# Kernel tuning notes

Measured on AMD Instinct MI355X. Metric: run time of the kernel, lower is better.

Reference implementation:

```python
import jax, jax.numpy as jnp
import numpy as np

N = 20000       # total atoms
E = 320000      # edges (avg degree 16)
F = 128         # num_features
R = 32          # num_radial
NB = 3          # num_blocks
CUTOFF = 5.0
MAX_Z = 37      # max_atomic_number + 1
MIN_DIST = 0.3
PI = 3.141592653589793


def swish(x):
    return x * jax.nn.sigmoid(x)


def sph_harm_l2(rhat):
    # Real spherical harmonics lmax=2, e3nn ordering, 'component' normalization.
    x, y, z = rhat[:, 0], rhat[:, 1], rhat[:, 2]
    s3, s5, s15 = 1.7320508075688772, 2.23606797749979, 3.872983346207417
    sh1 = jnp.stack([s3 * y, s3 * z, s3 * x], axis=-1)                    # l=1 (odd)
    sh2 = jnp.stack([s15 * x * y, s15 * y * z, 0.5 * s5 * (3.0 * z * z - 1.0),
                     s15 * z * x, 0.5 * s15 * (x * x - y * y)], axis=-1)  # l=2 (even)
    return sh1, sh2


def setup_inputs() -> dict:
    key = jax.random.key(0)
    ks = jax.random.split(key, 16)
    rn = lambda k, shape, scale: jax.random.normal(k, shape, dtype=jnp.float32) * scale
    inp = {}
    inp["z"] = jax.random.randint(ks[0], (N,), 0, MAX_Z)
    inp["pos"] = rn(ks[1], (N, 3), 3.0)
    inp["edge_index"] = jax.random.randint(ks[2], (2, E), 0, N)
    # embedding params
    inp["emb_table"] = rn(ks[3], (MAX_Z, F), 1.0)
    inp["emb_W"] = rn(ks[4], (F, F), F ** -0.5)
    inp["emb_b"] = jnp.zeros((F,), jnp.float32)
    # trainable Bessel frequencies (init n*pi, as in bessel RBF)
    inp["bessel_freq"] = jnp.arange(1, R + 1, dtype=jnp.float32) * PI
    # per-block params, stacked over NB blocks
    inp["Wf1"] = rn(ks[5], (NB, R, F), R ** -0.5)
    inp["bf1"] = jnp.zeros((NB, F), jnp.float32)
    inp["Wf2"] = rn(ks[6], (NB, F, 4 * F), F ** -0.5)
    inp["Wsrc"] = rn(ks[7], (NB, F, F), F ** -0.5)
    inp["Wu"] = rn(ks[8], (NB, F, 3 * F), F ** -0.5)
    inp["W1o"] = rn(ks[9], (NB, F, F), F ** -0.5)
    inp["W1e"] = rn(ks[10], (NB, F, F), F ** -0.5)
    inp["W2e"] = rn(ks[11], (NB, F, F), F ** -0.5)
    inp["Wup"] = rn(ks[12], (NB, 4 * F, F), (4 * F) ** -0.5)
    return inp


def forward(z, pos, edge_index, emb_table, emb_W, emb_b, bessel_freq,
            Wf1, bf1, Wf2, Wsrc, Wu, W1o, W1e, W2e, Wup):
    i, j = edge_index[0], edge_index[1]
    rij = pos[j] - pos[i]                                   # [E,3]
    r = jnp.sqrt(jnp.sum(rij * rij, axis=-1) + 1e-12)       # [E]
    rhat = rij / (r[:, None] + 1e-6)
    # mask replaces the edge filtering (min_distance and radius cutoff)
    edge_mask = ((r >= MIN_DIST) & (r < CUTOFF)).astype(pos.dtype)
    sh1, sh2 = sph_harm_l2(rhat)                            # [E,3], [E,5]
    # trainable Bessel RBF with cosine cutoff envelope
    fc = 0.5 * (jnp.cos(PI * r / CUTOFF) + 1.0) * edge_mask
    rbf = jnp.sqrt(2.0 / CUTOFF) * jnp.sin(bessel_freq[None, :] * r[:, None] / CUTOFF) / (r[:, None] + 1e-6)
    rbf = rbf * fc[:, None]                                 # [E,R]
    # atom embedding
    S = swish(emb_table[z] @ emb_W + emb_b)                 # [N,F]
    T = jnp.zeros((N, 11, F), S.dtype)                      # 1o(3)+1e(3)+2e(5) x F channels
    for b in range(NB):
        # radial filter network -> per-edge gates
        w = swish(rbf @ Wf1[b] + bf1[b]) @ Wf2[b]           # [E,4F]
        w = w * edge_mask[:, None]
        wS, w1, w2, w3 = jnp.split(w, 4, axis=-1)
        Sj = S[j]                                           # [E,F] gather
        # scalar messages
        mS = wS * swish(Sj @ Wsrc[b])                       # [E,F]
        aggS = jax.ops.segment_sum(mS, i, num_segments=N)   # [N,F]
        # equivariant messages: sh(l) outer-product edge features
        u1, u2, u3 = jnp.split(Sj @ Wu[b], 3, axis=-1)
        m1o = sh1[:, :, None] * (w1 * u1)[:, None, :]       # [E,3,F]
        m1e = sh1[:, :, None] * (w2 * u2)[:, None, :]       # [E,3,F]
        m2e = sh2[:, :, None] * (w3 * u3)[:, None, :]       # [E,5,F]
        mT = jnp.concatenate([m1o, m1e, m2e], axis=1)       # [E,11,F]
        aggT = jax.ops.segment_sum(mT, i, num_segments=N)   # [N,11,F] scatter-add
        Tin = T + aggT
        # per-irrep channel mixing (self-interaction)
        T1o = jnp.einsum('nmf,fg->nmg', Tin[:, 0:3], W1o[b])
        T1e = jnp.einsum('nmf,fg->nmg', Tin[:, 3:6], W1e[b])
        T2e = jnp.einsum('nmf,fg->nmg', Tin[:, 6:11], W2e[b])
        T = jnp.concatenate([T1o, T1e, T2e], axis=1)
        # invariant norms of each irrep feed back into scalar track
        inv = jnp.concatenate([jnp.sum(T1o * T1o, 1), jnp.sum(T1e * T1e, 1),
                               jnp.sum(T2e * T2e, 1)], axis=-1)   # [N,3F]
        S = S + swish(jnp.concatenate([aggS, inv], axis=-1) @ Wup[b])
    return S, T.reshape(N, 11 * F)


def reference(z, pos, edge_index, emb_table, emb_W, emb_b, bessel_freq,
              Wf1, bf1, Wf2, Wsrc, Wu, W1o, W1e, W2e, Wup):
    return forward(z, pos, edge_index, emb_table, emb_W, emb_b, bessel_freq,
                   Wf1, bf1, Wf2, Wsrc, Wu, W1o, W1e, W2e, Wup)
```

## Files before the change

kernel.cpp:

```cpp
#include <hip/hip_runtime.h>
#include <cstdint>
#include <cstddef>

#define NN 20000
#define EE 320000
#define FF 128
#define RR 32
#define MTE 16

typedef float  f32x4  __attribute__((ext_vector_type(4)));
typedef short  bf16x8 __attribute__((ext_vector_type(8)));

__device__ __forceinline__ float swishf(float x) {
    return x / (1.f + __expf(-x));
}
__device__ __forceinline__ unsigned short f2bf(float f) {
    unsigned int u = __builtin_bit_cast(unsigned int, f);
    u = (u + 0x7FFFu + ((u >> 16) & 1u)) >> 16;
    return (unsigned short)u;
}
__device__ __forceinline__ float bf2f(unsigned short h) {
    unsigned int u = ((unsigned int)h) << 16;
    return __builtin_bit_cast(float, u);
}

__global__ __launch_bounds__(256) void geom_deg_kernel(
    const float* __restrict__ pos, const int* __restrict__ eidx,
    int* __restrict__ deg)
{
    int e = blockIdx.x * 256 + threadIdx.x;
    if (e >= EE) return;
    int i = eidx[e], j = eidx[EE + e];
    float dx = pos[3*j+0] - pos[3*i+0];
    float dy = pos[3*j+1] - pos[3*i+1];
    float dz = pos[3*j+2] - pos[3*i+2];
    float r = sqrtf(dx*dx + dy*dy + dz*dz + 1e-12f);
    if (r >= 0.3f && r < 5.0f) atomicAdd(&deg[i], 1);
}

__global__ __launch_bounds__(256) void scan_kernel(
    const int* __restrict__ deg, int* __restrict__ cursor, int* __restrict__ cnt)
{
    __shared__ int part[256];
    const int t = threadIdx.x;
    const int lo = t * 79;
    const int hi = min(lo + 79, NN);
    int s = 0;
    for (int k = lo; k < hi; k++) s += deg[k];
    part[t] = s;
    __syncthreads();
    for (int off = 1; off < 256; off <<= 1) {
        int v = (t >= off) ? part[t - off] : 0;
        __syncthreads();
        part[t] += v;
        __syncthreads();
    }
    int run = (t == 0) ? 0 : part[t - 1];
    for (int k = lo; k < hi; k++) { cursor[k] = run; run += deg[k]; }
    if (t == 255) cnt[0] = part[255];
}

__global__ __launch_bounds__(256) void geom_scatter_kernel(
    const float* __restrict__ pos, const int* __restrict__ eidx,
    const float* __restrict__ freq, int* __restrict__ cursor,
    int* __restrict__ ei, int* __restrict__ ej,
    float* __restrict__ sh, unsigned short* __restrict__ rbfq)
{
    int e = blockIdx.x * 256 + threadIdx.x;
    if (e >= EE) return;
    int i = eidx[e], j = eidx[EE + e];
    float dx = pos[3*j+0] - pos[3*i+0];
    float dy = pos[3*j+1] - pos[3*i+1];
    float dz = pos[3*j+2] - pos[3*i+2];
    float r = sqrtf(dx*dx + dy*dy + dz*dz + 1e-12f);
    if (!(r >= 0.3f && r < 5.0f)) return;
    int slot = atomicAdd(&cursor[i], 1);
    ei[slot] = i; ej[slot] = j;
    float ir = 1.f / (r + 1e-6f);
    float x = dx*ir, y = dy*ir, z = dz*ir;
    const float s3 = 1.7320508075688772f, s5 = 2.23606797749979f, s15 = 3.872983346207417f;
    float* shp = sh + (size_t)slot * 8;
    shp[0] = s3*y; shp[1] = s3*z; shp[2] = s3*x;
    shp[3] = s15*x*y; shp[4] = s15*y*z; shp[5] = 0.5f*s5*(3.f*z*z - 1.f);
    shp[6] = s15*z*x; shp[7] = 0.5f*s15*(x*x - y*y);
    float fc = 0.5f * (cosf(3.14159265358979323846f * r * 0.2f) + 1.f);
    float pref = 0.6324555320336759f * fc * ir;
    unsigned short* rp = rbfq + (size_t)slot * RR;
    for (int k = 0; k < RR; k++) rp[k] = f2bf(pref * sinf(freq[k] * r * 0.2f));
}

__global__ __launch_bounds__(128) void embed_kernel(
    const int* __restrict__ z, const float* __restrict__ emb_table,
    const float* __restrict__ emb_W, const float* __restrict__ emb_b,
    float* __restrict__ S)
{
    int n = blockIdx.x;
    int f = threadIdx.x;
    __shared__ float row[FF];
    row[f] = emb_table[(size_t)z[n]*FF + f];
    __syncthreads();
    float acc = emb_b[f];
    for (int k = 0; k < FF; k++) acc += row[k] * emb_W[k*FF + f];
    S[(size_t)n*FF + f] = swishf(acc);
}

__global__ __launch_bounds__(256) void pack_kernel(
    const float* __restrict__ W1o, const float* __restrict__ W1e,
    const float* __restrict__ W2e, const float* __restrict__ Wup,
    unsigned short* __restrict__ ph, unsigned short* __restrict__ pl)
{
    int t = blockIdx.x * 256 + threadIdx.x;
    if (t >= 3 * 14336) return;
    int b = t / 14336, r = t % 14336;
    const float* src; int nks; size_t dstoff;
    if (r < 6144) {
        int mat = r / 2048, rr = r % 2048;
        src = (mat == 0 ? W1o : mat == 1 ? W1e : W2e) + (size_t)b * 16384;
        nks = 4;
        dstoff = (size_t)b * 114688 + (size_t)mat * 16384 + (size_t)rr * 8;
        r = rr;
    } else {
        int rr = r - 6144;
        src = Wup + (size_t)b * 65536;
        nks = 16;
        dstoff = (size_t)b * 114688 + 49152 + (size_t)rr * 8;
        r = rr;
    }
    int lane = r & 63;
    int fi = r >> 6;
    int ks = fi % nks, ct = fi / nks;
    int col = ct * 16 + (lane & 15);
    int kb = ks * 32 + (lane >> 4) * 8;
    #pragma unroll
    for (int e = 0; e < 8; e++) {
        float v = src[(size_t)(kb + e) * 128 + col];
        unsigned short h = f2bf(v);
        ph[dstoff + e] = h;
        pl[dstoff + e] = f2bf(v - bf2f(h));
    }
}

__global__ __launch_bounds__(256) void pack_pu_kernel(
    const float* __restrict__ Wsrc, const float* __restrict__ Wu,
    unsigned short* __restrict__ packPU)
{
    int t = blockIdx.x * 256 + threadIdx.x;
    if (t >= 3 * 8192) return;
    int b = t / 8192, r = t % 8192;
    int lane = r & 63, fi = r >> 6;
    int ks = fi & 3, ct = fi >> 2;
    int kb = ks * 32 + (lane >> 4) * 8;
    int colq = lane & 15;
    const float* src; int col, stride;
    if (ct < 8) { src = Wsrc + (size_t)b * 16384; col = ct*16 + colq; stride = 128; }
    else        { src = Wu   + (size_t)b * 49152; col = (ct-8)*16 + colq; stride = 384; }
    size_t dst = (size_t)b * 65536 + (size_t)fi * 512 + (size_t)lane * 8;
    #pragma unroll
    for (int e = 0; e < 8; e++)
        packPU[dst + e] = f2bf(src[(size_t)(kb + e) * stride + col]);
}

__global__ __launch_bounds__(256) void pack_f2_kernel(
    const float* __restrict__ Wf2, unsigned short* __restrict__ packF2)
{
    int t = blockIdx.x * 256 + threadIdx.x;
    if (t >= 3 * 8192) return;
    int b = t / 8192, r = t % 8192;
    int lane = r & 63, fi = r >> 6;
    int ks = fi & 3, ct = fi >> 2;
    int kb = ks * 32 + (lane >> 4) * 8;
    int col = ct * 16 + (lane & 15);
    const float* src = Wf2 + (size_t)b * 65536;
    size_t dst = (size_t)b * 65536 + (size_t)fi * 512 + (size_t)lane * 8;
    #pragma unroll
    for (int e = 0; e < 8; e++)
        packF2[dst + e] = f2bf(src[(size_t)(kb + e) * 512 + col]);
}

__global__ __launch_bounds__(256) void proj_kernel(
    const float* __restrict__ S, const unsigned short* __restrict__ packPU,
    unsigned short* __restrict__ PU)
{
    __shared__ float stage[16][132];
    const int tid = threadIdx.x;
    const int n0 = blockIdx.x * 16;

    for (int idx = tid; idx < 512; idx += 256) {
        int row = idx >> 5, k4 = (idx & 31) << 2;
        *(float4*)&stage[row][k4] = *(const float4*)&S[((size_t)(n0 + row) << 7) + k4];
    }
    __syncthreads();

    const int lane = tid & 63;
    const int wid  = tid >> 6;
    const int row  = lane & 15;
    const int k0   = (lane >> 4) * 8;

    f32x4 acc[8];
    #pragma unroll
    for (int c = 0; c < 8; c++) acc[c] = (f32x4){0.f, 0.f, 0.f, 0.f};

    #pragma unroll
    for (int ks = 0; ks < 4; ks++) {
        const float* sp = &stage[row][ks*32 + k0];
        bf16x8 a;
        #pragma unroll
        for (int e = 0; e < 8; e++) a[e] = (short)f2bf(sp[e]);
        #pragma unroll
        for (int cti = 0; cti < 8; cti++) {
            int ct = wid * 8 + cti;
            bf16x8 b = *(const bf16x8*)(packPU + (((size_t)ct * 4 + ks) * 64 + lane) * 8);
            acc[cti] = __builtin_amdgcn_mfma_f32_16x16x32_bf16(a, b, acc[cti], 0, 0, 0);
        }
    }

    #pragma unroll
    for (int cti = 0; cti < 8; cti++) {
        int ct = wid * 8 + cti;
        int col = ct * 16 + (lane & 15);
        #pragma unroll
        for (int q = 0; q < 4; q++) {
            int n = n0 + (lane >> 4) * 4 + q;
            float v = acc[cti][q];
            if (ct < 8) v = swishf(v);
            PU[(size_t)n * 512 + col] = f2bf(v);
        }
    }
}

__global__ __launch_bounds__(256) void msg_kernel(
    const int* __restrict__ cnt,
    const int* __restrict__ ei, const int* __restrict__ ej,
    const float* __restrict__ sh, const unsigned short* __restrict__ rbfq,
    const float* __restrict__ Wf1, const float* __restrict__ bf1,
    const unsigned short* __restrict__ packF2, const unsigned short* __restrict__ PU,
    float* __restrict__ aggS, float* __restrict__ aggT)
{
    const int Ea = cnt[0];
    const int base = blockIdx.x * MTE;
    if (base >= Ea) return;
    const int nval = min(MTE, Ea - base);
    const int tid = threadIdx.x;

    __shared__ float          rbf_s[MTE][RR];
    __shared__ unsigned short h_s[MTE][FF];
    __shared__ unsigned short w_s[MTE][512];
    __shared__ float          sh_s[MTE][8];
    __shared__ int            i_s[MTE];
    __shared__ int            j_s[MTE];

    if (tid < MTE) {
        i_s[tid] = (tid < nval) ? ei[base + tid] : -1;
        j_s[tid] = (tid < nval) ? ej[base + tid] : 0;
    }
    if (tid >= 64 && tid < 64 + MTE*8) {
        int t = tid - 64, e = t >> 3;
        sh_s[e][t & 7] = (e < nval) ? sh[(size_t)(base + e)*8 + (t & 7)] : 0.f;
    }
    for (int t = tid; t < MTE*RR; t += 256) {
        int e = t >> 5, k = t & 31;
        rbf_s[e][k] = (e < nval) ? bf2f(rbfq[(size_t)(base + e)*RR + k]) : 0.f;
    }
    __syncthreads();

    {
        const int f = tid & 127, eh = tid >> 7;
        float hacc[8];
        float bb = bf1[f];
        #pragma unroll
        for (int k = 0; k < 8; k++) hacc[k] = bb;
        for (int r = 0; r < RR; r++) {
            float wv = Wf1[r*FF + f];
            #pragma unroll
            for (int k = 0; k < 8; k++) hacc[k] += rbf_s[eh*8 + k][r] * wv;
        }
        #pragma unroll
        for (int k = 0; k < 8; k++) h_s[eh*8 + k][f] = f2bf(swishf(hacc[k]));
    }
    __syncthreads();

    {
        const int lane = tid & 63;
        const int wid  = tid >> 6;
        const int ra   = lane & 15;
        const int k0   = (lane >> 4) * 8;
        f32x4 acc[8];
        #pragma unroll
        for (int c = 0; c < 8; c++) acc[c] = (f32x4){0.f, 0.f, 0.f, 0.f};
        #pragma unroll
        for (int ks = 0; ks < 4; ks++) {
            bf16x8 a = *(const bf16x8*)&h_s[ra][ks*32 + k0];
            #pragma unroll
            for (int cti = 0; cti < 8; cti++) {
                int ct = wid * 8 + cti;
                bf16x8 b = *(const bf16x8*)(packF2 + (((size_t)ct * 4 + ks) * 64 + lane) * 8);
                acc[cti] = __builtin_amdgcn_mfma_f32_16x16x32_bf16(a, b, acc[cti], 0, 0, 0);
            }
        }
        #pragma unroll
        for (int cti = 0; cti < 8; cti++) {
            int ct = wid * 8 + cti;
            int col = ct * 16 + (lane & 15);
            #pragma unroll
            for (int q = 0; q < 4; q++)
                w_s[(lane >> 4)*4 + q][col] = f2bf(acc[cti][q]);
        }
    }
    __syncthreads();

    const int f = tid & 127;
    if (tid < 128) {
        float aS = 0.f, a3 = 0.f, a4 = 0.f, a5 = 0.f;
        int cur = i_s[0];
        for (int e = 0; e < nval; e++) {
            int ie = i_s[e];
            if (ie != cur) {
                atomicAdd(&aggS[((size_t)cur << 7) + f], aS);
                size_t bT = (((size_t)cur*11 + 3) << 7) + f;
                atomicAdd(&aggT[bT], a3); atomicAdd(&aggT[bT + 128], a4); atomicAdd(&aggT[bT + 256], a5);
                aS = a3 = a4 = a5 = 0.f; cur = ie;
            }
            const unsigned short* pu = PU + (size_t)j_s[e] * 512;
            float wS = bf2f(w_s[e][f]),       P  = bf2f(pu[f]);
            float w2 = bf2f(w_s[e][256 + f]), U2 = bf2f(pu[256 + f]);
            aS += wS * P;
            float v = w2 * U2;
            a3 += sh_s[e][0]*v; a4 += sh_s[e][1]*v; a5 += sh_s[e][2]*v;
        }
        atomicAdd(&aggS[((size_t)cur << 7) + f], aS);
        size_t bT = (((size_t)cur*11 + 3) << 7) + f;
        atomicAdd(&aggT[bT], a3); atomicAdd(&aggT[bT + 128], a4); atomicAdd(&aggT[bT + 256], a5);
    } else {
        float a0 = 0.f, a1 = 0.f, a2 = 0.f;
        float a6 = 0.f, a7 = 0.f, a8 = 0.f, a9 = 0.f, a10 = 0.f;
        int cur = i_s[0];
        for (int e = 0; e < nval; e++) {
            int ie = i_s[e];
            if (ie != cur) {
                size_t bT = (((size_t)cur*11) << 7) + f;
                atomicAdd(&aggT[bT], a0); atomicAdd(&aggT[bT + 128], a1); atomicAdd(&aggT[bT + 256], a2);
                size_t bT2 = (((size_t)cur*11 + 6) << 7) + f;
                atomicAdd(&aggT[bT2], a6); atomicAdd(&aggT[bT2 + 128], a7); atomicAdd(&aggT[bT2 + 256], a8);
                atomicAdd(&aggT[bT2 + 384], a9); atomicAdd(&aggT[bT2 + 512], a10);
                a0 = a1 = a2 = a6 = a7 = a8 = a9 = a10 = 0.f; cur = ie;
            }
            const unsigned short* pu = PU + (size_t)j_s[e] * 512;
            float w1 = bf2f(w_s[e][128 + f]), U1 = bf2f(pu[128 + f]);
            float w3 = bf2f(w_s[e][384 + f]), U3 = bf2f(pu[384 + f]);
            float v1 = w1 * U1;
            a0 += sh_s[e][0]*v1; a1 += sh_s[e][1]*v1; a2 += sh_s[e][2]*v1;
            float v3 = w3 * U3;
            a6 += sh_s[e][3]*v3; a7 += sh_s[e][4]*v3; a8 += sh_s[e][5]*v3;
            a9 += sh_s[e][6]*v3; a10 += sh_s[e][7]*v3;
        }
        size_t bT = (((size_t)cur*11) << 7) + f;
        atomicAdd(&aggT[bT], a0); atomicAdd(&aggT[bT + 128], a1); atomicAdd(&aggT[bT + 256], a2);
        size_t bT2 = (((size_t)cur*11 + 6) << 7) + f;
        atomicAdd(&aggT[bT2], a6); atomicAdd(&aggT[bT2 + 128], a7); atomicAdd(&aggT[bT2 + 256], a8);
        atomicAdd(&aggT[bT2 + 384], a9); atomicAdd(&aggT[bT2 + 512], a10);
    }
}

template<int GSIZE>
__global__ __launch_bounds__(256) void tgemm_kernel(
    const float* __restrict__ aggT,
    const unsigned short* __restrict__ Wh, const unsigned short* __restrict__ Wl,
    float* __restrict__ T, float* __restrict__ inv,
    int goff, int invoff, int addT)
{
    __shared__ float stage[GSIZE][16][132];
    const int tid = threadIdx.x;
    const int n0 = blockIdx.x * 16;

    const int total = GSIZE * 16 * 32;
    for (int idx = tid; idx < total; idx += 256) {
        int mg  = idx >> 9;
        int rem = idx & 511;
        int row = rem >> 5;
        int k4  = (rem & 31) << 2;
        size_t g = (((size_t)(n0 + row) * 11 + goff + mg) << 7) + k4;
        float4 v = *(const float4*)&aggT[g];
        if (addT) {
            float4 tv = *(const float4*)&T[g];
            v.x += tv.x; v.y += tv.y; v.z += tv.z; v.w += tv.w;
        }
        *(float4*)&stage[mg][row][k4] = v;
    }
    __syncthreads();

    const int lane = tid & 63;
    const int wid  = tid >> 6;
    const int row  = lane & 15;
    const int k0   = (lane >> 4) * 8;

    f32x4 acc[GSIZE][2];
    #pragma unroll
    for (int mg = 0; mg < GSIZE; mg++) {
        acc[mg][0] = (f32x4){0.f, 0.f, 0.f, 0.f};
        acc[mg][1] = (f32x4){0.f, 0.f, 0.f, 0.f};
    }

    #pragma unroll
    for (int ks = 0; ks < 4; ks++) {
        bf16x8 ah[GSIZE], al[GSIZE];
        #pragma unroll
        for (int mg = 0; mg < GSIZE; mg++) {
            const float* sp = &stage[mg][row][ks*32 + k0];
            float v0[4], v1[4];
            *(float4*)v0 = *(const float4*)sp;
            *(float4*)v1 = *(const float4*)(sp + 4);
            #pragma unroll
            for (int e = 0; e < 4; e++) {
                unsigned short h0 = f2bf(v0[e]);
                ah[mg][e]   = (short)h0;
                al[mg][e]   = (short)f2bf(v0[e] - bf2f(h0));
                unsigned short h1 = f2bf(v1[e]);
                ah[mg][4+e] = (short)h1;
                al[mg][4+e] = (short)f2bf(v1[e] - bf2f(h1));
            }
        }
        #pragma unroll
        for (int cti = 0; cti < 2; cti++) {
            const int ct = wid * 2 + cti;
            size_t boff = (((size_t)ct * 4 + ks) * 64 + lane) * 8;
            bf16x8 bh = *(const bf16x8*)(Wh + boff);
            bf16x8 bl = *(const bf16x8*)(Wl + boff);
            #pragma unroll
            for (int mg = 0; mg < GSIZE; mg++) {
                acc[mg][cti] = __builtin_amdgcn_mfma_f32_16x16x32_bf16(ah[mg], bh, acc[mg][cti], 0, 0, 0);
                acc[mg][cti] = __builtin_amdgcn_mfma_f32_16x16x32_bf16(al[mg], bh, acc[mg][cti], 0, 0, 0);
                acc[mg][cti] = __builtin_amdgcn_mfma_f32_16x16x32_bf16(ah[mg], bl, acc[mg][cti], 0, 0, 0);
            }
        }
    }

    #pragma unroll
    for (int cti = 0; cti < 2; cti++) {
        const int ct = wid * 2 + cti;
        const int fc = ct * 16 + (lane & 15);
        #pragma unroll
        for (int q = 0; q < 4; q++) {
            const int n = n0 + (lane >> 4) * 4 + q;
            float iv = 0.f;
            #pragma unroll
            for (int mg = 0; mg < GSIZE; mg++) {
                float o = acc[mg][cti][q];
                T[(((size_t)n * 11 + goff + mg) << 7) + fc] = o;
                iv += o * o;
            }
            inv[(size_t)n * 384 + invoff + fc] = iv;
        }
    }
}

__global__ __launch_bounds__(256) void sgemm2_kernel(
    const float* __restrict__ aggS, const float* __restrict__ inv,
    const unsigned short* __restrict__ Wh, const unsigned short* __restrict__ Wl,
    float* __restrict__ S)
{
    __shared__ float stage[16][516];
    const int tid = threadIdx.x;
    const int n0 = blockIdx.x * 16;

    for (int idx = tid; idx < 16 * 128; idx += 256) {
        int row = idx >> 7;
        int k4  = (idx & 127) << 2;
        float4 v;
        if (k4 < 128) v = *(const float4*)&aggS[((size_t)(n0 + row) << 7) + k4];
        else          v = *(const float4*)&inv[(size_t)(n0 + row) * 384 + (k4 - 128)];
        *(float4*)&stage[row][k4] = v;
    }
    __syncthreads();

    const int lane = tid & 63;
    const int wid  = tid >> 6;
    const int row  = lane & 15;
    const int k0   = (lane >> 4) * 8;

    f32x4 acc[2];
    acc[0] = (f32x4){0.f, 0.f, 0.f, 0.f};
    acc[1] = (f32x4){0.f, 0.f, 0.f, 0.f};

    for (int ks = 0; ks < 16; ks++) {
        const float* sp = &stage[row][ks*32 + k0];
        float v0[4], v1[4];
        *(float4*)v0 = *(const float4*)sp;
        *(float4*)v1 = *(const float4*)(sp + 4);
        bf16x8 ah, al;
        #pragma unroll
        for (int e = 0; e < 4; e++) {
            unsigned short h0 = f2bf(v0[e]);
            ah[e]   = (short)h0;
            al[e]   = (short)f2bf(v0[e] - bf2f(h0));
            unsigned short h1 = f2bf(v1[e]);
            ah[4+e] = (short)h1;
            al[4+e] = (short)f2bf(v1[e] - bf2f(h1));
        }
        #pragma unroll
        for (int cti = 0; cti < 2; cti++) {
            const int ct = wid * 2 + cti;
            size_t boff = (((size_t)ct * 16 + ks) * 64 + lane) * 8;
            bf16x8 bh = *(const bf16x8*)(Wh + boff);
            bf16x8 bl = *(const bf16x8*)(Wl + boff);
            acc[cti] = __builtin_amdgcn_mfma_f32_16x16x32_bf16(ah, bh, acc[cti], 0, 0, 0);
            acc[cti] = __builtin_amdgcn_mfma_f32_16x16x32_bf16(al, bh, acc[cti], 0, 0, 0);
            acc[cti] = __builtin_amdgcn_mfma_f32_16x16x32_bf16(ah, bl, acc[cti], 0, 0, 0);
        }
    }

    #pragma unroll
    for (int cti = 0; cti < 2; cti++) {
        const int ct = wid * 2 + cti;
        const int fc = ct * 16 + (lane & 15);
        #pragma unroll
        for (int q = 0; q < 4; q++) {
            const int n = n0 + (lane >> 4) * 4 + q;
            size_t o = ((size_t)n << 7) + fc;
            S[o] += swishf(acc[cti][q]);
        }
    }
}

extern "C" void kernel_launch(void* const* d_in, const int* in_sizes, int n_in,
                              void* d_out, int out_size, void* d_ws, size_t ws_size,
                              hipStream_t stream)
{
    const int*   z         = (const int*)  d_in[0];
    const float* pos       = (const float*)d_in[1];
    const int*   eidx      = (const int*)  d_in[2];
    const float* emb_table = (const float*)d_in[3];
    const float* emb_W     = (const float*)d_in[4];
    const float* emb_b     = (const float*)d_in[5];
    const float* freq      = (const float*)d_in[6];
    const float* Wf1       = (const float*)d_in[7];
    const float* bf1       = (const float*)d_in[8];
    const float* Wf2       = (const float*)d_in[9];
    const float* Wsrc      = (const float*)d_in[10];
    const float* Wu        = (const float*)d_in[11];
    const float* W1o       = (const float*)d_in[12];
    const float* W1e       = (const float*)d_in[13];
    const float* W2e       = (const float*)d_in[14];
    const float* Wup       = (const float*)d_in[15];

    float* S = (float*)d_out;
    float* T = S + (size_t)NN*FF;

    char* w = (char*)d_ws;
    int*   cnt    = (int*)w;                      w += 256;
    int*   deg    = (int*)w;                      w += (size_t)NN*4 + 128;
    int*   cursor = (int*)w;                      w += (size_t)NN*4 + 128;
    int*   ei     = (int*)w;                      w += (size_t)EE*4;
    int*   ej     = (int*)w;                      w += (size_t)EE*4;
    float* sh     = (float*)w;                    w += (size_t)EE*8*4;
    unsigned short* rbfq = (unsigned short*)w;    w += (size_t)EE*RR*2;
    unsigned short* PU   = (unsigned short*)w;    w += (size_t)NN*512*2;
    float* aggS   = (float*)w;                    w += (size_t)NN*FF*4;
    float* aggT   = (float*)w;                    w += (size_t)NN*11*FF*4;
    float* inv    = (float*)w;                    w += (size_t)NN*384*4;
    unsigned short* packH  = (unsigned short*)w;  w += (size_t)344064*2;
    unsigned short* packL  = (unsigned short*)w;  w += (size_t)344064*2;
    unsigned short* packPU = (unsigned short*)w;  w += (size_t)3*65536*2;
    unsigned short* packF2 = (unsigned short*)w;  w += (size_t)3*65536*2;

    hipMemsetAsync(deg, 0, (size_t)NN*4, stream);

    geom_deg_kernel<<<(EE + 255)/256, 256, 0, stream>>>(pos, eidx, deg);
    scan_kernel<<<1, 256, 0, stream>>>(deg, cursor, cnt);
    geom_scatter_kernel<<<(EE + 255)/256, 256, 0, stream>>>(pos, eidx, freq, cursor, ei, ej, sh, rbfq);
    embed_kernel<<<NN, 128, 0, stream>>>(z, emb_table, emb_W, emb_b, S);
    pack_kernel<<<(3*14336 + 255)/256, 256, 0, stream>>>(W1o, W1e, W2e, Wup, packH, packL);
    pack_pu_kernel<<<(3*8192 + 255)/256, 256, 0, stream>>>(Wsrc, Wu, packPU);
    pack_f2_kernel<<<(3*8192 + 255)/256, 256, 0, stream>>>(Wf2, packF2);

    for (int b = 0; b < 3; b++) {
        hipMemsetAsync(aggS, 0, (size_t)NN*FF*4 + (size_t)NN*11*FF*4, stream);
        proj_kernel<<<NN/16, 256, 0, stream>>>(S, packPU + (size_t)b*65536, PU);
        msg_kernel<<<(EE + MTE - 1)/MTE, 256, 0, stream>>>(
            cnt, ei, ej, sh, rbfq,
            Wf1 + (size_t)b*RR*FF, bf1 + (size_t)b*FF,
            packF2 + (size_t)b*65536, PU, aggS, aggT);

        const unsigned short* H = packH + (size_t)b*114688;
        const unsigned short* L = packL + (size_t)b*114688;
        tgemm_kernel<3><<<NN/16, 256, 0, stream>>>(aggT, H +     0, L +     0, T, inv, 0,   0, b > 0);
        tgemm_kernel<3><<<NN/16, 256, 0, stream>>>(aggT, H + 16384, L + 16384, T, inv, 3, 128, b > 0);
        tgemm_kernel<5><<<NN/16, 256, 0, stream>>>(aggT, H + 32768, L + 32768, T, inv, 6, 256, b > 0);
        sgemm2_kernel<<<NN/16, 256, 0, stream>>>(aggS, inv, H + 49152, L + 49152, S);
    }
}
```

Measured before the change: 985.2 us.

## Segment edges per destination node, replace atomics with stores, fuse projection into sgemm2

The message kernel now assigns each block a fixed group of destination nodes through a CSR start array and walks only their sorted edges. Each node's sum is built in registers and written with plain stores, which removes the float atomics and the per-block memset of the aggregation buffers. Nodes with no edges are zeroed explicitly. PU is stored interleaved (four values per feature) so one 8-byte load fetches all four, and the next block's source projection is fused into sgemm2's epilogue, dropping the separate proj launches. The risk is load imbalance, since blocks with high-degree nodes loop longer, and fewer blocks run overall.

```diff
diff --git a/kernel.cpp b/kernel.cpp
--- a/kernel.cpp
+++ b/kernel.cpp
@@ -7,6 +7,7 @@
 #define FF 128
 #define RR 32
 #define MTE 16
+#define NPB 4
 
 typedef float  f32x4  __attribute__((ext_vector_type(4)));
 typedef short  bf16x8 __attribute__((ext_vector_type(8)));
@@ -39,7 +40,7 @@
 }
 
 __global__ __launch_bounds__(256) void scan_kernel(
-    const int* __restrict__ deg, int* __restrict__ cursor, int* __restrict__ cnt)
+    const int* __restrict__ deg, int* __restrict__ cursor, int* __restrict__ cstart)
 {
     __shared__ int part[256];
     const int t = threadIdx.x;
@@ -56,8 +57,8 @@
         __syncthreads();
     }
     int run = (t == 0) ? 0 : part[t - 1];
-    for (int k = lo; k < hi; k++) { cursor[k] = run; run += deg[k]; }
-    if (t == 255) cnt[0] = part[255];
+    for (int k = lo; k < hi; k++) { cursor[k] = run; cstart[k] = run; run += deg[k]; }
+    if (t == 255) cstart[NN] = run;
 }
 
 __global__ __launch_bounds__(256) void geom_scatter_kernel(
@@ -217,147 +218,177 @@
     #pragma unroll
     for (int cti = 0; cti < 8; cti++) {
         int ct = wid * 8 + cti;
-        int col = ct * 16 + (lane & 15);
+        int cblk = ct >> 3;
+        int fcol = (ct & 7) * 16 + (lane & 15);
         #pragma unroll
         for (int q = 0; q < 4; q++) {
             int n = n0 + (lane >> 4) * 4 + q;
             float v = acc[cti][q];
-            if (ct < 8) v = swishf(v);
-            PU[(size_t)n * 512 + col] = f2bf(v);
+            if (cblk == 0) v = swishf(v);
+            PU[(size_t)n * 512 + fcol * 4 + cblk] = f2bf(v);
         }
     }
 }
 
 __global__ __launch_bounds__(256) void msg_kernel(
-    const int* __restrict__ cnt,
+    const int* __restrict__ cstart,
     const int* __restrict__ ei, const int* __restrict__ ej,
     const float* __restrict__ sh, const unsigned short* __restrict__ rbfq,
     const float* __restrict__ Wf1, const float* __restrict__ bf1,
     const unsigned short* __restrict__ packF2, const unsigned short* __restrict__ PU,
     float* __restrict__ aggS, float* __restrict__ aggT)
 {
-    const int Ea = cnt[0];
-    const int base = blockIdx.x * MTE;
-    if (base >= Ea) return;
-    const int nval = min(MTE, Ea - base);
+    const int n0 = blockIdx.x * NPB;
+    const int estart = cstart[n0];
+    const int eend   = cstart[n0 + NPB];
     const int tid = threadIdx.x;
+    const int f = tid & 127;
+    const int half = tid >> 7;
+    const int lane = tid & 63;
+    const int wid  = tid >> 6;
 
     __shared__ float          rbf_s[MTE][RR];
     __shared__ unsigned short h_s[MTE][FF];
-    __shared__ unsigned short w_s[MTE][512];
+    __shared__ unsigned short w_s[MTE][520];
     __shared__ float          sh_s[MTE][8];
-    __shared__ int            i_s[MTE];
-    __shared__ int            j_s[MTE];
-
-    if (tid < MTE) {
-        i_s[tid] = (tid < nval) ? ei[base + tid] : -1;
-        j_s[tid] = (tid < nval) ? ej[base + tid] : 0;
-    }
-    if (tid >= 64 && tid < 64 + MTE*8) {
-        int t = tid - 64, e = t >> 3;
-        sh_s[e][t & 7] = (e < nval) ? sh[(size_t)(base + e)*8 + (t & 7)] : 0.f;
-    }
-    for (int t = tid; t < MTE*RR; t += 256) {
-        int e = t >> 5, k = t & 31;
-        rbf_s[e][k] = (e < nval) ? bf2f(rbfq[(size_t)(base + e)*RR + k]) : 0.f;
-    }
-    __syncthreads();
-
-    {
-        const int f = tid & 127, eh = tid >> 7;
-        float hacc[8];
-        float bb = bf1[f];
-        #pragma unroll
-        for (int k = 0; k < 8; k++) hacc[k] = bb;
-        for (int r = 0; r < RR; r++) {
-            float wv = Wf1[r*FF + f];
-            #pragma unroll
-            for (int k = 0; k < 8; k++) hacc[k] += rbf_s[eh*8 + k][r] * wv;
-        }
-        #pragma unroll
-        for (int k = 0; k < 8; k++) h_s[eh*8 + k][f] = f2bf(swishf(hacc[k]));
-    }
-    __syncthreads();
-
-    {
-        const int lane = tid & 63;
-        const int wid  = tid >> 6;
-        const int ra   = lane & 15;
-        const int k0   = (lane >> 4) * 8;
-        f32x4 acc[8];
-        #pragma unroll
-        for (int c = 0; c < 8; c++) acc[c] = (f32x4){0.f, 0.f, 0.f, 0.f};
-        #pragma unroll
-        for (int ks = 0; ks < 4; ks++) {
-            bf16x8 a = *(const bf16x8*)&h_s[ra][ks*32 + k0];
+    __shared__ int            i_s[MTE], j_s[MTE];
+
+    float aS=0.f, a3=0.f, a4=0.f, a5=0.f;
+    float a0=0.f,a1=0.f,a2=0.f,a6=0.f,a7=0.f,a8=0.f,a9=0.f,a10=0.f;
+    int cur = -1;
+
+    for (int eoff = estart; eoff < eend; eoff += MTE) {
+        const int te = min(MTE, eend - eoff);
+        __syncthreads();
+        if (tid < MTE) {
+            i_s[tid] = (tid < te) ? ei[eoff + tid] : -1;
+            j_s[tid] = (tid < te) ? ej[eoff + tid] : 0;
+        }
+        if (tid >= 64 && tid < 64 + MTE*8) {
+            int t = tid - 64, e = t >> 3;
+            sh_s[e][t & 7] = (e < te) ? sh[(size_t)(eoff + e)*8 + (t & 7)] : 0.f;
+        }
+        for (int t = tid; t < MTE*RR; t += 256) {
+            int e = t >> 5, k = t & 31;
+            rbf_s[e][k] = (e < te) ? bf2f(rbfq[(size_t)(eoff + e)*RR + k]) : 0.f;
+        }
+        __syncthreads();
+        if (cur < 0) cur = i_s[0];
+
+        {
+            float hacc[8];
+            float bb = bf1[f];
+            #pragma unroll
+            for (int k = 0; k < 8; k++) hacc[k] = bb;
+            for (int r = 0; r < RR; r++) {
+                float wv = Wf1[r*FF + f];
+                #pragma unroll
+                for (int k = 0; k < 8; k++) hacc[k] += rbf_s[half*8 + k][r] * wv;
+            }
+            #pragma unroll
+            for (int k = 0; k < 8; k++)
+                h_s[half*8 + k][f] = f2bf(swishf(hacc[k]));
+        }
+        __syncthreads();
+
+        {
+            const int ra = lane & 15, k0 = (lane >> 4) * 8;
+            f32x4 wacc[8];
+            #pragma unroll
+            for (int c = 0; c < 8; c++) wacc[c] = (f32x4){0.f, 0.f, 0.f, 0.f};
+            #pragma unroll
+            for (int ks = 0; ks < 4; ks++) {
+                bf16x8 a = *(const bf16x8*)&h_s[ra][ks*32 + k0];
+                #pragma unroll
+                for (int cti = 0; cti < 8; cti++) {
+                    int ct = wid * 8 + cti;
+                    bf16x8 b = *(const bf16x8*)(packF2 + (((size_t)ct * 4 + ks) * 64 + lane) * 8);
+                    wacc[cti] = __builtin_amdgcn_mfma_f32_16x16x32_bf16(a, b, wacc[cti], 0, 0, 0);
+                }
+            }
             #pragma unroll
             for (int cti = 0; cti < 8; cti++) {
                 int ct = wid * 8 + cti;
-                bf16x8 b = *(const bf16x8*)(packF2 + (((size_t)ct * 4 + ks) * 64 + lane) * 8);
-                acc[cti] = __builtin_amdgcn_mfma_f32_16x16x32_bf16(a, b, acc[cti], 0, 0, 0);
-            }
-        }
-        #pragma unroll
-        for (int cti = 0; cti < 8; cti++) {
-            int ct = wid * 8 + cti;
-            int col = ct * 16 + (lane & 15);
-            #pragma unroll
-            for (int q = 0; q < 4; q++)
-                w_s[(lane >> 4)*4 + q][col] = f2bf(acc[cti][q]);
-        }
-    }
-    __syncthreads();
-
-    const int f = tid & 127;
-    if (tid < 128) {
-        float aS = 0.f, a3 = 0.f, a4 = 0.f, a5 = 0.f;
-        int cur = i_s[0];
-        for (int e = 0; e < nval; e++) {
+                int cblk = ct >> 3;
+                int fcol = (ct & 7) * 16 + (lane & 15);
+                #pragma unroll
+                for (int q = 0; q < 4; q++)
+                    w_s[(lane >> 4)*4 + q][fcol*4 + cblk] = f2bf(wacc[cti][q]);
+            }
+        }
+        __syncthreads();
+
+        uint2 puv[MTE];
+        #pragma unroll
+        for (int e = 0; e < MTE; e++)
+            puv[e] = *(const uint2*)(PU + ((size_t)j_s[e] << 9) + (f << 2));
+
+        #pragma unroll
+        for (int e = 0; e < MTE; e++) {
+            if (e >= te) break;
             int ie = i_s[e];
             if (ie != cur) {
-                atomicAdd(&aggS[((size_t)cur << 7) + f], aS);
-                size_t bT = (((size_t)cur*11 + 3) << 7) + f;
-                atomicAdd(&aggT[bT], a3); atomicAdd(&aggT[bT + 128], a4); atomicAdd(&aggT[bT + 256], a5);
-                aS = a3 = a4 = a5 = 0.f; cur = ie;
-            }
-            const unsigned short* pu = PU + (size_t)j_s[e] * 512;
-            float wS = bf2f(w_s[e][f]),       P  = bf2f(pu[f]);
-            float w2 = bf2f(w_s[e][256 + f]), U2 = bf2f(pu[256 + f]);
-            aS += wS * P;
-            float v = w2 * U2;
-            a3 += sh_s[e][0]*v; a4 += sh_s[e][1]*v; a5 += sh_s[e][2]*v;
-        }
-        atomicAdd(&aggS[((size_t)cur << 7) + f], aS);
-        size_t bT = (((size_t)cur*11 + 3) << 7) + f;
-        atomicAdd(&aggT[bT], a3); atomicAdd(&aggT[bT + 128], a4); atomicAdd(&aggT[bT + 256], a5);
-    } else {
-        float a0 = 0.f, a1 = 0.f, a2 = 0.f;
-        float a6 = 0.f, a7 = 0.f, a8 = 0.f, a9 = 0.f, a10 = 0.f;
-        int cur = i_s[0];
-        for (int e = 0; e < nval; e++) {
-            int ie = i_s[e];
-            if (ie != cur) {
-                size_t bT = (((size_t)cur*11) << 7) + f;
-                atomicAdd(&aggT[bT], a0); atomicAdd(&aggT[bT + 128], a1); atomicAdd(&aggT[bT + 256], a2);
-                size_t bT2 = (((size_t)cur*11 + 6) << 7) + f;
-                atomicAdd(&aggT[bT2], a6); atomicAdd(&aggT[bT2 + 128], a7); atomicAdd(&aggT[bT2 + 256], a8);
-                atomicAdd(&aggT[bT2 + 384], a9); atomicAdd(&aggT[bT2 + 512], a10);
-                a0 = a1 = a2 = a6 = a7 = a8 = a9 = a10 = 0.f; cur = ie;
-            }
-            const unsigned short* pu = PU + (size_t)j_s[e] * 512;
-            float w1 = bf2f(w_s[e][128 + f]), U1 = bf2f(pu[128 + f]);
-            float w3 = bf2f(w_s[e][384 + f]), U3 = bf2f(pu[384 + f]);
-            float v1 = w1 * U1;
-            a0 += sh_s[e][0]*v1; a1 += sh_s[e][1]*v1; a2 += sh_s[e][2]*v1;
-            float v3 = w3 * U3;
-            a6 += sh_s[e][3]*v3; a7 += sh_s[e][4]*v3; a8 += sh_s[e][5]*v3;
-            a9 += sh_s[e][6]*v3; a10 += sh_s[e][7]*v3;
-        }
-        size_t bT = (((size_t)cur*11) << 7) + f;
-        atomicAdd(&aggT[bT], a0); atomicAdd(&aggT[bT + 128], a1); atomicAdd(&aggT[bT + 256], a2);
-        size_t bT2 = (((size_t)cur*11 + 6) << 7) + f;
-        atomicAdd(&aggT[bT2], a6); atomicAdd(&aggT[bT2 + 128], a7); atomicAdd(&aggT[bT2 + 256], a8);
-        atomicAdd(&aggT[bT2 + 384], a9); atomicAdd(&aggT[bT2 + 512], a10);
+                if (half == 0) {
+                    aggS[((size_t)cur << 7) + f] = aS;
+                    size_t bT = (((size_t)cur*11 + 3) << 7) + f;
+                    aggT[bT] = a3; aggT[bT + 128] = a4; aggT[bT + 256] = a5;
+                    aS = a3 = a4 = a5 = 0.f;
+                } else {
+                    size_t bT = (((size_t)cur*11) << 7) + f;
+                    aggT[bT] = a0; aggT[bT + 128] = a1; aggT[bT + 256] = a2;
+                    size_t bT2 = (((size_t)cur*11 + 6) << 7) + f;
+                    aggT[bT2] = a6; aggT[bT2 + 128] = a7; aggT[bT2 + 256] = a8;
+                    aggT[bT2 + 384] = a9; aggT[bT2 + 512] = a10;
+                    a0=a1=a2=a6=a7=a8=a9=a10=0.f;
+                }
+                cur = ie;
+            }
+            uint2 wv2 = *(const uint2*)&w_s[e][f*4];
+            uint2 pv  = puv[e];
+            if (half == 0) {
+                float wS = bf2f((unsigned short)(wv2.x & 0xffff));
+                float w2 = bf2f((unsigned short)(wv2.y & 0xffff));
+                float P  = bf2f((unsigned short)(pv.x  & 0xffff));
+                float U2 = bf2f((unsigned short)(pv.y  & 0xffff));
+                aS += wS * P;
+                float v = w2 * U2;
+                a3 += sh_s[e][0]*v; a4 += sh_s[e][1]*v; a5 += sh_s[e][2]*v;
+            } else {
+                float w1 = bf2f((unsigned short)(wv2.x >> 16));
+                float w3 = bf2f((unsigned short)(wv2.y >> 16));
+                float U1 = bf2f((unsigned short)(pv.x  >> 16));
+                float U3 = bf2f((unsigned short)(pv.y  >> 16));
+                float v1 = w1 * U1;
+                a0 += sh_s[e][0]*v1; a1 += sh_s[e][1]*v1; a2 += sh_s[e][2]*v1;
+                float v3 = w3 * U3;
+                a6 += sh_s[e][3]*v3; a7 += sh_s[e][4]*v3; a8 += sh_s[e][5]*v3;
+                a9 += sh_s[e][6]*v3; a10 += sh_s[e][7]*v3;
+            }
+        }
+    }
+    if (cur >= 0) {
+        if (half == 0) {
+            aggS[((size_t)cur << 7) + f] = aS;
+            size_t bT = (((size_t)cur*11 + 3) << 7) + f;
+            aggT[bT] = a3; aggT[bT + 128] = a4; aggT[bT + 256] = a5;
+        } else {
+            size_t bT = (((size_t)cur*11) << 7) + f;
+            aggT[bT] = a0; aggT[bT + 128] = a1; aggT[bT + 256] = a2;
+            size_t bT2 = (((size_t)cur*11 + 6) << 7) + f;
+            aggT[bT2] = a6; aggT[bT2 + 128] = a7; aggT[bT2 + 256] = a8;
+            aggT[bT2 + 384] = a9; aggT[bT2 + 512] = a10;
+        }
+    }
+    #pragma unroll
+    for (int ln = 0; ln < NPB; ln++) {
+        int n = n0 + ln;
+        if (cstart[n + 1] == cstart[n]) {
+            for (int idx = tid; idx < 12*128; idx += 256) {
+                int row = idx >> 7, ff = idx & 127;
+                if (row == 0) aggS[((size_t)n << 7) + ff] = 0.f;
+                else aggT[(((size_t)n*11 + row - 1) << 7) + ff] = 0.f;
+            }
+        }
     }
 }
 
@@ -456,9 +487,11 @@
 __global__ __launch_bounds__(256) void sgemm2_kernel(
     const float* __restrict__ aggS, const float* __restrict__ inv,
     const unsigned short* __restrict__ Wh, const unsigned short* __restrict__ Wl,
-    float* __restrict__ S)
+    const unsigned short* __restrict__ packPUn,
+    float* __restrict__ S, unsigned short* __restrict__ PU, int doPU)
 {
     __shared__ float stage[16][516];
+    __shared__ float snew[16][132];
     const int tid = threadIdx.x;
     const int n0 = blockIdx.x * 16;
 
@@ -516,7 +549,44 @@
         for (int q = 0; q < 4; q++) {
             const int n = n0 + (lane >> 4) * 4 + q;
             size_t o = ((size_t)n << 7) + fc;
-            S[o] += swishf(acc[cti][q]);
+            float sv = S[o] + swishf(acc[cti][q]);
+            S[o] = sv;
+            snew[(lane >> 4)*4 + q][fc] = sv;
+        }
+    }
+
+    if (!doPU) return;
+    __syncthreads();
+
+    {
+        f32x4 pacc[8];
+        #pragma unroll
+        for (int c = 0; c < 8; c++) pacc[c] = (f32x4){0.f, 0.f, 0.f, 0.f};
+        #pragma unroll
+        for (int ks = 0; ks < 4; ks++) {
+            bf16x8 a;
+            #pragma unroll
+            for (int e = 0; e < 8; e++)
+                a[e] = (short)f2bf(snew[row][ks*32 + k0 + e]);
+            #pragma unroll
+            for (int cti = 0; cti < 8; cti++) {
+                int ct = wid * 8 + cti;
+                bf16x8 b = *(const bf16x8*)(packPUn + (((size_t)ct * 4 + ks) * 64 + lane) * 8);
+                pacc[cti] = __builtin_amdgcn_mfma_f32_16x16x32_bf16(a, b, pacc[cti], 0, 0, 0);
+            }
+        }
+        #pragma unroll
+        for (int cti = 0; cti < 8; cti++) {
+            int ct = wid * 8 + cti;
+            int cblk = ct >> 3;
+            int fcol = (ct & 7) * 16 + (lane & 15);
+            #pragma unroll
+            for (int q = 0; q < 4; q++) {
+                int n = n0 + (lane >> 4) * 4 + q;
+                float v = pacc[cti][q];
+                if (cblk == 0) v = swishf(v);
+                PU[((size_t)n << 9) + fcol*4 + cblk] = f2bf(v);
+            }
         }
     }
 }
@@ -546,9 +616,9 @@
     float* T = S + (size_t)NN*FF;
 
     char* w = (char*)d_ws;
-    int*   cnt    = (int*)w;                      w += 256;
     int*   deg    = (int*)w;                      w += (size_t)NN*4 + 128;
     int*   cursor = (int*)w;                      w += (size_t)NN*4 + 128;
+    int*   cstart = (int*)w;                      w += (size_t)(NN+1)*4 + 124;
     int*   ei     = (int*)w;                      w += (size_t)EE*4;
     int*   ej     = (int*)w;                      w += (size_t)EE*4;
     float* sh     = (float*)w;                    w += (size_t)EE*8*4;
@@ -565,18 +635,18 @@
     hipMemsetAsync(deg, 0, (size_t)NN*4, stream);
 
     geom_deg_kernel<<<(EE + 255)/256, 256, 0, stream>>>(pos, eidx, deg);
-    scan_kernel<<<1, 256, 0, stream>>>(deg, cursor, cnt);
+    scan_kernel<<<1, 256, 0, stream>>>(deg, cursor, cstart);
     geom_scatter_kernel<<<(EE + 255)/256, 256, 0, stream>>>(pos, eidx, freq, cursor, ei, ej, sh, rbfq);
     embed_kernel<<<NN, 128, 0, stream>>>(z, emb_table, emb_W, emb_b, S);
     pack_kernel<<<(3*14336 + 255)/256, 256, 0, stream>>>(W1o, W1e, W2e, Wup, packH, packL);
     pack_pu_kernel<<<(3*8192 + 255)/256, 256, 0, stream>>>(Wsrc, Wu, packPU);
     pack_f2_kernel<<<(3*8192 + 255)/256, 256, 0, stream>>>(Wf2, packF2);
 
+    proj_kernel<<<NN/16, 256, 0, stream>>>(S, packPU, PU);
+
     for (int b = 0; b < 3; b++) {
-        hipMemsetAsync(aggS, 0, (size_t)NN*FF*4 + (size_t)NN*11*FF*4, stream);
-        proj_kernel<<<NN/16, 256, 0, stream>>>(S, packPU + (size_t)b*65536, PU);
-        msg_kernel<<<(EE + MTE - 1)/MTE, 256, 0, stream>>>(
-            cnt, ei, ej, sh, rbfq,
+        msg_kernel<<<NN/NPB, 256, 0, stream>>>(
+            cstart, ei, ej, sh, rbfq,
             Wf1 + (size_t)b*RR*FF, bf1 + (size_t)b*FF,
             packF2 + (size_t)b*65536, PU, aggS, aggT);
 
@@ -585,6 +655,9 @@
         tgemm_kernel<3><<<NN/16, 256, 0, stream>>>(aggT, H +     0, L +     0, T, inv, 0,   0, b > 0);
         tgemm_kernel<3><<<NN/16, 256, 0, stream>>>(aggT, H + 16384, L + 16384, T, inv, 3, 128, b > 0);
         tgemm_kernel<5><<<NN/16, 256, 0, stream>>>(aggT, H + 32768, L + 32768, T, inv, 6, 256, b > 0);
-        sgemm2_kernel<<<NN/16, 256, 0, stream>>>(aggS, inv, H + 49152, L + 49152, S);
-    }
-}
+        sgemm2_kernel<<<NN/16, 256, 0, stream>>>(
+            aggS, inv, H + 49152, L + 49152,
+            packPU + (size_t)(b < 2 ? (b+1)*65536 : 0),
+            S, PU, b < 2);
+    }
+}
```

Result: slower. 1.599 ms (+62.3%).

## Interleave PU/W channels and use plain stores for block-interior node segments

Applied to the files above, without the earlier changes.

Changes the PU and per-edge weight layouts so the four channel groups of a feature are adjacent, letting each thread fetch all four bf16 values with one 8-byte load. Keeps per-node start offsets from the scan so the message kernel can see when a node's whole edge segment lies inside one block, and then writes its aggregate with plain stores instead of atomics. Pads the shared weight tile to reduce bank conflicts. Each thread now loads values belonging to the other half, and the plain-store path depends on the memset zeroing and on CSR offsets being correct.

```diff
diff --git a/kernel.cpp b/kernel.cpp
--- a/kernel.cpp
+++ b/kernel.cpp
@@ -39,7 +39,7 @@
 }
 
 __global__ __launch_bounds__(256) void scan_kernel(
-    const int* __restrict__ deg, int* __restrict__ cursor, int* __restrict__ cnt)
+    const int* __restrict__ deg, int* __restrict__ cursor, int* __restrict__ cstart)
 {
     __shared__ int part[256];
     const int t = threadIdx.x;
@@ -56,8 +56,8 @@
         __syncthreads();
     }
     int run = (t == 0) ? 0 : part[t - 1];
-    for (int k = lo; k < hi; k++) { cursor[k] = run; run += deg[k]; }
-    if (t == 255) cnt[0] = part[255];
+    for (int k = lo; k < hi; k++) { cursor[k] = run; cstart[k] = run; run += deg[k]; }
+    if (t == 255) cstart[NN] = part[255];
 }
 
 __global__ __launch_bounds__(256) void geom_scatter_kernel(
@@ -217,37 +217,41 @@
     #pragma unroll
     for (int cti = 0; cti < 8; cti++) {
         int ct = wid * 8 + cti;
-        int col = ct * 16 + (lane & 15);
+        int cblk = ct >> 3;
+        int fcol = (ct & 7) * 16 + (lane & 15);
         #pragma unroll
         for (int q = 0; q < 4; q++) {
             int n = n0 + (lane >> 4) * 4 + q;
             float v = acc[cti][q];
-            if (ct < 8) v = swishf(v);
-            PU[(size_t)n * 512 + col] = f2bf(v);
+            if (cblk == 0) v = swishf(v);
+            PU[(size_t)n * 512 + fcol * 4 + cblk] = f2bf(v);
         }
     }
 }
 
 __global__ __launch_bounds__(256) void msg_kernel(
-    const int* __restrict__ cnt,
+    const int* __restrict__ cstart,
     const int* __restrict__ ei, const int* __restrict__ ej,
     const float* __restrict__ sh, const unsigned short* __restrict__ rbfq,
     const float* __restrict__ Wf1, const float* __restrict__ bf1,
     const unsigned short* __restrict__ packF2, const unsigned short* __restrict__ PU,
     float* __restrict__ aggS, float* __restrict__ aggT)
 {
-    const int Ea = cnt[0];
+    const int Ea = cstart[NN];
     const int base = blockIdx.x * MTE;
     if (base >= Ea) return;
     const int nval = min(MTE, Ea - base);
     const int tid = threadIdx.x;
+    const int f = tid & 127;
+    const int half = tid >> 7;
+    const int lane = tid & 63;
+    const int wid  = tid >> 6;
 
     __shared__ float          rbf_s[MTE][RR];
     __shared__ unsigned short h_s[MTE][FF];
-    __shared__ unsigned short w_s[MTE][512];
+    __shared__ unsigned short w_s[MTE][520];
     __shared__ float          sh_s[MTE][8];
-    __shared__ int            i_s[MTE];
-    __shared__ int            j_s[MTE];
+    __shared__ int            i_s[MTE], j_s[MTE];
 
     if (tid < MTE) {
         i_s[tid] = (tid < nval) ? ei[base + tid] : -1;
@@ -264,7 +268,6 @@
     __syncthreads();
 
     {
-        const int f = tid & 127, eh = tid >> 7;
         float hacc[8];
         float bb = bf1[f];
         #pragma unroll
@@ -272,21 +275,19 @@
         for (int r = 0; r < RR; r++) {
             float wv = Wf1[r*FF + f];
             #pragma unroll
-            for (int k = 0; k < 8; k++) hacc[k] += rbf_s[eh*8 + k][r] * wv;
-        }
-        #pragma unroll
-        for (int k = 0; k < 8; k++) h_s[eh*8 + k][f] = f2bf(swishf(hacc[k]));
+            for (int k = 0; k < 8; k++) hacc[k] += rbf_s[half*8 + k][r] * wv;
+        }
+        #pragma unroll
+        for (int k = 0; k < 8; k++)
+            h_s[half*8 + k][f] = f2bf(swishf(hacc[k]));
     }
     __syncthreads();
 
     {
-        const int lane = tid & 63;
-        const int wid  = tid >> 6;
-        const int ra   = lane & 15;
-        const int k0   = (lane >> 4) * 8;
-        f32x4 acc[8];
-        #pragma unroll
-        for (int c = 0; c < 8; c++) acc[c] = (f32x4){0.f, 0.f, 0.f, 0.f};
+        const int ra = lane & 15, k0 = (lane >> 4) * 8;
+        f32x4 wacc[8];
+        #pragma unroll
+        for (int c = 0; c < 8; c++) wacc[c] = (f32x4){0.f, 0.f, 0.f, 0.f};
         #pragma unroll
         for (int ks = 0; ks < 4; ks++) {
             bf16x8 a = *(const bf16x8*)&h_s[ra][ks*32 + k0];
@@ -294,71 +295,82 @@
             for (int cti = 0; cti < 8; cti++) {
                 int ct = wid * 8 + cti;
                 bf16x8 b = *(const bf16x8*)(packF2 + (((size_t)ct * 4 + ks) * 64 + lane) * 8);
-                acc[cti] = __builtin_amdgcn_mfma_f32_16x16x32_bf16(a, b, acc[cti], 0, 0, 0);
+                wacc[cti] = __builtin_amdgcn_mfma_f32_16x16x32_bf16(a, b, wacc[cti], 0, 0, 0);
             }
         }
         #pragma unroll
         for (int cti = 0; cti < 8; cti++) {
             int ct = wid * 8 + cti;
-            int col = ct * 16 + (lane & 15);
+            int cblk = ct >> 3;
+            int fcol = (ct & 7) * 16 + (lane & 15);
             #pragma unroll
             for (int q = 0; q < 4; q++)
-                w_s[(lane >> 4)*4 + q][col] = f2bf(acc[cti][q]);
-        }
-    }
-    __syncthreads();
-
-    const int f = tid & 127;
-    if (tid < 128) {
-        float aS = 0.f, a3 = 0.f, a4 = 0.f, a5 = 0.f;
-        int cur = i_s[0];
-        for (int e = 0; e < nval; e++) {
-            int ie = i_s[e];
-            if (ie != cur) {
-                atomicAdd(&aggS[((size_t)cur << 7) + f], aS);
-                size_t bT = (((size_t)cur*11 + 3) << 7) + f;
+                w_s[(lane >> 4)*4 + q][fcol*4 + cblk] = f2bf(wacc[cti][q]);
+        }
+    }
+    __syncthreads();
+
+    float aS=0.f, a3=0.f, a4=0.f, a5=0.f;
+    float a0=0.f,a1=0.f,a2=0.f,a6=0.f,a7=0.f,a8=0.f,a9=0.f,a10=0.f;
+    int cur = i_s[0];
+
+    auto flush = [&](int node) {
+        bool interior = (cstart[node] >= base) && (cstart[node + 1] <= base + nval);
+        if (half == 0) {
+            size_t sA = ((size_t)node << 7) + f;
+            size_t bT = (((size_t)node*11 + 3) << 7) + f;
+            if (interior) {
+                aggS[sA] = aS;
+                aggT[bT] = a3; aggT[bT + 128] = a4; aggT[bT + 256] = a5;
+            } else {
+                atomicAdd(&aggS[sA], aS);
                 atomicAdd(&aggT[bT], a3); atomicAdd(&aggT[bT + 128], a4); atomicAdd(&aggT[bT + 256], a5);
-                aS = a3 = a4 = a5 = 0.f; cur = ie;
             }
-            const unsigned short* pu = PU + (size_t)j_s[e] * 512;
-            float wS = bf2f(w_s[e][f]),       P  = bf2f(pu[f]);
-            float w2 = bf2f(w_s[e][256 + f]), U2 = bf2f(pu[256 + f]);
+            aS = a3 = a4 = a5 = 0.f;
+        } else {
+            size_t bT  = (((size_t)node*11) << 7) + f;
+            size_t bT2 = (((size_t)node*11 + 6) << 7) + f;
+            if (interior) {
+                aggT[bT] = a0; aggT[bT + 128] = a1; aggT[bT + 256] = a2;
+                aggT[bT2] = a6; aggT[bT2 + 128] = a7; aggT[bT2 + 256] = a8;
+                aggT[bT2 + 384] = a9; aggT[bT2 + 512] = a10;
+            } else {
+                atomicAdd(&aggT[bT], a0); atomicAdd(&aggT[bT + 128], a1); atomicAdd(&aggT[bT + 256], a2);
+                atomicAdd(&aggT[bT2], a6); atomicAdd(&aggT[bT2 + 128], a7); atomicAdd(&aggT[bT2 + 256], a8);
+                atomicAdd(&aggT[bT2 + 384], a9); atomicAdd(&aggT[bT2 + 512], a10);
+            }
+            a0=a1=a2=a6=a7=a8=a9=a10=0.f;
+        }
+    };
+
+    #pragma unroll
+    for (int e = 0; e < MTE; e++) {
+        if (e >= nval) break;
+        int ie = i_s[e];
+        if (ie != cur) { flush(cur); cur = ie; }
+        uint2 wv2 = *(const uint2*)&w_s[e][f*4];
+        uint2 pv  = *(const uint2*)(PU + ((size_t)j_s[e] << 9) + (f << 2));
+        if (half == 0) {
+            float wS = bf2f((unsigned short)(wv2.x & 0xffff));
+            float w2 = bf2f((unsigned short)(wv2.y & 0xffff));
+            float P  = bf2f((unsigned short)(pv.x  & 0xffff));
+            float U2 = bf2f((unsigned short)(pv.y  & 0xffff));
             aS += wS * P;
             float v = w2 * U2;
             a3 += sh_s[e][0]*v; a4 += sh_s[e][1]*v; a5 += sh_s[e][2]*v;
-        }
-        atomicAdd(&aggS[((size_t)cur << 7) + f], aS);
-        size_t bT = (((size_t)cur*11 + 3) << 7) + f;
-        atomicAdd(&aggT[bT], a3); atomicAdd(&aggT[bT + 128], a4); atomicAdd(&aggT[bT + 256], a5);
-    } else {
-        float a0 = 0.f, a1 = 0.f, a2 = 0.f;
-        float a6 = 0.f, a7 = 0.f, a8 = 0.f, a9 = 0.f, a10 = 0.f;
-        int cur = i_s[0];
-        for (int e = 0; e < nval; e++) {
-            int ie = i_s[e];
-            if (ie != cur) {
-                size_t bT = (((size_t)cur*11) << 7) + f;
-                atomicAdd(&aggT[bT], a0); atomicAdd(&aggT[bT + 128], a1); atomicAdd(&aggT[bT + 256], a2);
-                size_t bT2 = (((size_t)cur*11 + 6) << 7) + f;
-                atomicAdd(&aggT[bT2], a6); atomicAdd(&aggT[bT2 + 128], a7); atomicAdd(&aggT[bT2 + 256], a8);
-                atomicAdd(&aggT[bT2 + 384], a9); atomicAdd(&aggT[bT2 + 512], a10);
-                a0 = a1 = a2 = a6 = a7 = a8 = a9 = a10 = 0.f; cur = ie;
-            }
-            const unsigned short* pu = PU + (size_t)j_s[e] * 512;
-            float w1 = bf2f(w_s[e][128 + f]), U1 = bf2f(pu[128 + f]);
-            float w3 = bf2f(w_s[e][384 + f]), U3 = bf2f(pu[384 + f]);
+        } else {
+            float w1 = bf2f((unsigned short)(wv2.x >> 16));
+            float w3 = bf2f((unsigned short)(wv2.y >> 16));
+            float U1 = bf2f((unsigned short)(pv.x  >> 16));
+            float U3 = bf2f((unsigned short)(pv.y  >> 16));
             float v1 = w1 * U1;
             a0 += sh_s[e][0]*v1; a1 += sh_s[e][1]*v1; a2 += sh_s[e][2]*v1;
             float v3 = w3 * U3;
             a6 += sh_s[e][3]*v3; a7 += sh_s[e][4]*v3; a8 += sh_s[e][5]*v3;
             a9 += sh_s[e][6]*v3; a10 += sh_s[e][7]*v3;
         }
-        size_t bT = (((size_t)cur*11) << 7) + f;
-        atomicAdd(&aggT[bT], a0); atomicAdd(&aggT[bT + 128], a1); atomicAdd(&aggT[bT + 256], a2);
-        size_t bT2 = (((size_t)cur*11 + 6) << 7) + f;
-        atomicAdd(&aggT[bT2], a6); atomicAdd(&aggT[bT2 + 128], a7); atomicAdd(&aggT[bT2 + 256], a8);
-        atomicAdd(&aggT[bT2 + 384], a9); atomicAdd(&aggT[bT2 + 512], a10);
-    }
+    }
+    flush(cur);
 }
 
 template<int GSIZE>
@@ -546,9 +558,9 @@
     float* T = S + (size_t)NN*FF;
 
     char* w = (char*)d_ws;
-    int*   cnt    = (int*)w;                      w += 256;
     int*   deg    = (int*)w;                      w += (size_t)NN*4 + 128;
     int*   cursor = (int*)w;                      w += (size_t)NN*4 + 128;
+    int*   cstart = (int*)w;                      w += (size_t)(NN+1)*4 + 124;
     int*   ei     = (int*)w;                      w += (size_t)EE*4;
     int*   ej     = (int*)w;                      w += (size_t)EE*4;
     float* sh     = (float*)w;                    w += (size_t)EE*8*4;
@@ -565,7 +577,7 @@
     hipMemsetAsync(deg, 0, (size_t)NN*4, stream);
 
     geom_deg_kernel<<<(EE + 255)/256, 256, 0, stream>>>(pos, eidx, deg);
-    scan_kernel<<<1, 256, 0, stream>>>(deg, cursor, cnt);
+    scan_kernel<<<1, 256, 0, stream>>>(deg, cursor, cstart);
     geom_scatter_kernel<<<(EE + 255)/256, 256, 0, stream>>>(pos, eidx, freq, cursor, ei, ej, sh, rbfq);
     embed_kernel<<<NN, 128, 0, stream>>>(z, emb_table, emb_W, emb_b, S);
     pack_kernel<<<(3*14336 + 255)/256, 256, 0, stream>>>(W1o, W1e, W2e, Wup, packH, packL);
@@ -576,7 +588,7 @@
         hipMemsetAsync(aggS, 0, (size_t)NN*FF*4 + (size_t)NN*11*FF*4, stream);
         proj_kernel<<<NN/16, 256, 0, stream>>>(S, packPU + (size_t)b*65536, PU);
         msg_kernel<<<(EE + MTE - 1)/MTE, 256, 0, stream>>>(
-            cnt, ei, ej, sh, rbfq,
+            cstart, ei, ej, sh, rbfq,
             Wf1 + (size_t)b*RR*FF, bf1 + (size_t)b*FF,
             packF2 + (size_t)b*65536, PU, aggS, aggT);
 
```

After: 998.2 us. About the same (+1.3%).
